# Kernel optimization log

Hardware: AMD Instinct MI355X
Metric: run time of the kernel (lower is better)

## Reference

```python
import jax, jax.numpy as jnp
import numpy as np

N_NODES = 50000
N_EDGES = 640000
D_IN = 128
D_OUT = 128


def setup_inputs() -> dict:
    key = jax.random.key(0)
    k1, k2, k3, k4, k5, k6 = jax.random.split(key, 6)
    nfeat = jax.random.normal(k1, (N_NODES, D_IN), dtype=jnp.float32)
    w = jax.random.uniform(k2, (N_EDGES,), dtype=jnp.float32)
    # nn.Linear weights are [out_feats, in_feats], Kaiming-uniform-ish scale
    bound = 1.0 / np.sqrt(D_IN)
    W1 = jax.random.uniform(k3, (D_OUT, D_IN), dtype=jnp.float32, minval=-bound, maxval=bound)
    W2 = jax.random.uniform(k4, (D_OUT, D_IN), dtype=jnp.float32, minval=-bound, maxval=bound)
    src = jax.random.randint(k5, (N_EDGES,), 0, N_NODES, dtype=jnp.int64)
    dst = jax.random.randint(k6, (N_EDGES,), 0, N_NODES, dtype=jnp.int64)
    return {"nfeat": nfeat, "w": w, "W1": W1, "W2": W2, "src": src, "dst": dst}


def reference(nfeat, w, W1, W2, src, dst):
    # feat_drop is identity in eval mode
    h = nfeat  # [N, D_IN]
    # update_all(u_mul_e('h','w','m'), sum('m','h_neighbor')):
    # gather source features, scale by per-edge scalar weight, scatter-sum to dst
    msg = h[src] * w[:, None]                                   # [E, D_IN]
    h_neighbor = jax.ops.segment_sum(msg, dst, num_segments=h.shape[0])  # [N, D_IN]
    # Bi-interaction residual: leaky_relu(Linear(h + hn)) + leaky_relu(Linear(h * hn))
    add_branch = jax.nn.leaky_relu((h + h_neighbor) @ W1.T, negative_slope=0.01)
    mul_branch = jax.nn.leaky_relu((h * h_neighbor) @ W2.T, negative_slope=0.01)
    out = add_branch + mul_branch                                # [N, D_OUT]
    return (h_neighbor, out)
```

## Files before the change

kernel.cpp:

```cpp
#include <hip/hip_runtime.h>
#include <hip/hip_bf16.h>

#define N_NODES 50000
#define N_EDGES 640000
#define D 128
#define OUT0_ELEMS (N_NODES * D)
#define SCAN_BLOCKS ((N_NODES + 255) / 256)

typedef __attribute__((ext_vector_type(8))) short short8v;
typedef __attribute__((ext_vector_type(4))) short short4v;
typedef __attribute__((ext_vector_type(4))) float f32x4;

static __device__ __forceinline__ unsigned short f2bf(float x) {
  __hip_bfloat16 b = __float2bfloat16(x);
  return *reinterpret_cast<unsigned short*>(&b);
}
static __device__ __forceinline__ float bf2f(unsigned short u) {
  unsigned x = ((unsigned)u) << 16;
  return __builtin_bit_cast(float, x);
}
static __device__ __forceinline__ unsigned pack_edge(int s, float wv) {
  return ((unsigned)f2bf(wv) << 16) | (unsigned)s;
}

__global__ __launch_bounds__(256) void conv_all(
    const float* __restrict__ nfeat, const float* __restrict__ W1,
    const float* __restrict__ W2, unsigned short* __restrict__ nf16,
    unsigned short* __restrict__ wc, int* __restrict__ cnt) {
  int i = blockIdx.x * 256 + threadIdx.x;
  int base = i * 8;
  float4 a = *(const float4*)(nfeat + base);
  float4 b = *(const float4*)(nfeat + base + 4);
  short8v o;
  o[0] = (short)f2bf(a.x); o[1] = (short)f2bf(a.y);
  o[2] = (short)f2bf(a.z); o[3] = (short)f2bf(a.w);
  o[4] = (short)f2bf(b.x); o[5] = (short)f2bf(b.y);
  o[6] = (short)f2bf(b.z); o[7] = (short)f2bf(b.w);
  *(short8v*)(nf16 + base) = o;
  if (i < D * D) {
    wc[i] = f2bf(W1[i]);
    wc[D * D + i] = f2bf(W2[i]);
  }
  if (i < N_NODES) cnt[i] = 0;
}

__global__ __launch_bounds__(256) void hist_rank(
    const int* __restrict__ dst, int* __restrict__ cnt, int* __restrict__ rank) {
  int t = blockIdx.x * 256 + threadIdx.x;
  int e = t * 4;
  if (e >= N_EDGES) return;
  int4 d4 = *(const int4*)(dst + e);
  int4 r4;
  r4.x = atomicAdd(&cnt[d4.x], 1);
  r4.y = atomicAdd(&cnt[d4.y], 1);
  r4.z = atomicAdd(&cnt[d4.z], 1);
  r4.w = atomicAdd(&cnt[d4.w], 1);
  *(int4*)(rank + e) = r4;
}

__global__ __launch_bounds__(256) void scan_block(
    const int* __restrict__ cnt, int* __restrict__ offs, int* __restrict__ bsums) {
  __shared__ int sdata[256];
  int t = threadIdx.x;
  int i = blockIdx.x * 256 + t;
  int v = (i < N_NODES) ? cnt[i] : 0;
  sdata[t] = v;
  __syncthreads();
#pragma unroll
  for (int off = 1; off < 256; off <<= 1) {
    int x = (t >= off) ? sdata[t - off] : 0;
    __syncthreads();
    sdata[t] += x;
    __syncthreads();
  }
  if (i < N_NODES) offs[i] = sdata[t] - v;
  if (t == 255) bsums[blockIdx.x] = sdata[t];
}

__global__ __launch_bounds__(256) void scan_fin(
    int* __restrict__ offs, const int* __restrict__ bsums) {
  __shared__ int sdata[256];
  int t = threadIdx.x;
  int v = (t < SCAN_BLOCKS) ? bsums[t] : 0;
  sdata[t] = v;
  __syncthreads();
#pragma unroll
  for (int off = 1; off < 256; off <<= 1) {
    int x = (t >= off) ? sdata[t - off] : 0;
    __syncthreads();
    sdata[t] += x;
    __syncthreads();
  }
  int prefix = (blockIdx.x > 0) ? sdata[blockIdx.x - 1] : 0;
  int i = blockIdx.x * 256 + t;
  if (i < N_NODES) offs[i] += prefix;
  if (i == N_NODES - 1) offs[N_NODES] = N_EDGES;
}

__global__ __launch_bounds__(256) void fill4(
    const int* __restrict__ src, const int* __restrict__ dst,
    const float* __restrict__ w, const int* __restrict__ rank,
    const int* __restrict__ offs, unsigned* __restrict__ es) {
  int t = blockIdx.x * 256 + threadIdx.x;
  int e = t * 4;
  if (e >= N_EDGES) return;
  int4 d4 = *(const int4*)(dst + e);
  int4 r4 = *(const int4*)(rank + e);
  int4 s4 = *(const int4*)(src + e);
  float4 w4 = *(const float4*)(w + e);
  es[offs[d4.x] + r4.x] = pack_edge(s4.x, w4.x);
  es[offs[d4.y] + r4.y] = pack_edge(s4.y, w4.y);
  es[offs[d4.z] + r4.z] = pack_edge(s4.z, w4.z);
  es[offs[d4.w] + r4.w] = pack_edge(s4.w, w4.w);
}

__global__ __launch_bounds__(256) void gather_bf16(
    const unsigned short* __restrict__ nf16, const int* __restrict__ offs,
    const unsigned* __restrict__ es, float* __restrict__ hn) {
  int tid = blockIdx.x * 256 + threadIdx.x;
  int node = tid >> 4;
  if (node >= N_NODES) return;
  int q = tid & 15;
  int beg = offs[node];
  int end = offs[node + 1];
  float acc[8];
#pragma unroll
  for (int j = 0; j < 8; ++j) acc[j] = 0.f;

  int k = beg;
  for (; k + 3 < end; k += 4) {
    unsigned r0 = es[k], r1 = es[k + 1], r2 = es[k + 2], r3 = es[k + 3];
    short8v v0 = *(const short8v*)(nf16 + (size_t)(r0 & 0xFFFF) * D + q * 8);
    short8v v1 = *(const short8v*)(nf16 + (size_t)(r1 & 0xFFFF) * D + q * 8);
    short8v v2 = *(const short8v*)(nf16 + (size_t)(r2 & 0xFFFF) * D + q * 8);
    short8v v3 = *(const short8v*)(nf16 + (size_t)(r3 & 0xFFFF) * D + q * 8);
    float w0 = bf2f((unsigned short)(r0 >> 16));
    float w1 = bf2f((unsigned short)(r1 >> 16));
    float w2 = bf2f((unsigned short)(r2 >> 16));
    float w3 = bf2f((unsigned short)(r3 >> 16));
#pragma unroll
    for (int j = 0; j < 8; ++j) {
      acc[j] += bf2f((unsigned short)v0[j]) * w0;
      acc[j] += bf2f((unsigned short)v1[j]) * w1;
      acc[j] += bf2f((unsigned short)v2[j]) * w2;
      acc[j] += bf2f((unsigned short)v3[j]) * w3;
    }
  }
  for (; k < end; ++k) {
    unsigned r0 = es[k];
    short8v v0 = *(const short8v*)(nf16 + (size_t)(r0 & 0xFFFF) * D + q * 8);
    float w0 = bf2f((unsigned short)(r0 >> 16));
#pragma unroll
    for (int j = 0; j < 8; ++j) acc[j] += bf2f((unsigned short)v0[j]) * w0;
  }

  float* orow = hn + (size_t)node * D + q * 8;
  *(float4*)(orow) = make_float4(acc[0], acc[1], acc[2], acc[3]);
  *(float4*)(orow + 4) = make_float4(acc[4], acc[5], acc[6], acc[7]);
}

__global__ __launch_bounds__(256) void bi_mfma_h16(
    const unsigned short* __restrict__ h16, const float* __restrict__ hn,
    const unsigned short* __restrict__ wc, float* __restrict__ out) {
  __shared__ __align__(16) unsigned short lds[2 * 64 * D];

  const int tid = threadIdx.x;
  const int lane = tid & 63;
  const int wid = tid >> 6;
  const int base = blockIdx.x * 64;
  const int r16 = lane & 15;
  const int kg = lane >> 4;

  short8v bf[2][2][4];
  {
    const int colbase = wid * 32;
#pragma unroll
    for (int g = 0; g < 2; ++g)
#pragma unroll
      for (int c = 0; c < 2; ++c)
#pragma unroll
        for (int ks = 0; ks < 4; ++ks) {
          int col = colbase + c * 16 + r16;
          int k = ks * 32 + kg * 8;
          bf[g][c][ks] =
              *(const short8v*)(wc + (size_t)g * D * D + (size_t)col * D + k);
        }
  }

#pragma unroll
  for (int p = 0; p < 8; ++p) {
    int flat = p * 1024 + tid * 4;
    int row = flat >> 7;
    int col = flat & 127;
    int node = base + row;
    float hx0 = 0.f, hx1 = 0.f, hx2 = 0.f, hx3 = 0.f;
    float4 nv = make_float4(0.f, 0.f, 0.f, 0.f);
    if (node < N_NODES) {
      short4v hv = *(const short4v*)(h16 + (size_t)node * D + col);
      hx0 = bf2f((unsigned short)hv[0]);
      hx1 = bf2f((unsigned short)hv[1]);
      hx2 = bf2f((unsigned short)hv[2]);
      hx3 = bf2f((unsigned short)hv[3]);
      nv = *(const float4*)(hn + (size_t)node * D + col);
    }
    short4v av, mv;
    av[0] = (short)f2bf(hx0 + nv.x);
    av[1] = (short)f2bf(hx1 + nv.y);
    av[2] = (short)f2bf(hx2 + nv.z);
    av[3] = (short)f2bf(hx3 + nv.w);
    mv[0] = (short)f2bf(hx0 * nv.x);
    mv[1] = (short)f2bf(hx1 * nv.y);
    mv[2] = (short)f2bf(hx2 * nv.z);
    mv[3] = (short)f2bf(hx3 * nv.w);
    int boff = (row * 256 + col * 2) ^ ((row & 7) << 4);
    *(short4v*)((char*)lds + boff) = av;
    *(short4v*)((char*)lds + 16384 + boff) = mv;
  }
  __syncthreads();

  f32x4 acc1[4][2], acc2[4][2];
#pragma unroll
  for (int rt = 0; rt < 4; ++rt)
#pragma unroll
    for (int c = 0; c < 2; ++c) {
      acc1[rt][c] = (f32x4){0.f, 0.f, 0.f, 0.f};
      acc2[rt][c] = (f32x4){0.f, 0.f, 0.f, 0.f};
    }

#pragma unroll
  for (int ks = 0; ks < 4; ++ks) {
#pragma unroll
    for (int rt = 0; rt < 4; ++rt) {
      int row = rt * 16 + r16;
      int boff = (row * 256 + (ks * 32 + kg * 8) * 2) ^ ((row & 7) << 4);
      short8v a1 = *(const short8v*)((const char*)lds + boff);
      short8v a2 = *(const short8v*)((const char*)lds + 16384 + boff);
#pragma unroll
      for (int c = 0; c < 2; ++c) {
        acc1[rt][c] = __builtin_amdgcn_mfma_f32_16x16x32_bf16(
            a1, bf[0][c][ks], acc1[rt][c], 0, 0, 0);
        acc2[rt][c] = __builtin_amdgcn_mfma_f32_16x16x32_bf16(
            a2, bf[1][c][ks], acc2[rt][c], 0, 0, 0);
      }
    }
  }

#pragma unroll
  for (int rt = 0; rt < 4; ++rt) {
#pragma unroll
    for (int c = 0; c < 2; ++c) {
#pragma unroll
      for (int e = 0; e < 4; ++e) {
        int row = rt * 16 + kg * 4 + e;
        int node = base + row;
        if (node < N_NODES) {
          int col = wid * 32 + c * 16 + r16;
          float x1 = acc1[rt][c][e];
          float x2 = acc2[rt][c][e];
          x1 = x1 > 0.f ? x1 : 0.01f * x1;
          x2 = x2 > 0.f ? x2 : 0.01f * x2;
          out[(size_t)node * D + col] = x1 + x2;
        }
      }
    }
  }
}

__global__ __launch_bounds__(256) void edge_scatter(
    const float* __restrict__ nfeat, const float* __restrict__ w,
    const int* __restrict__ src, const int* __restrict__ dst,
    float* __restrict__ hn) {
  int tid = blockIdx.x * 256 + threadIdx.x;
  int e = tid >> 5;
  if (e >= N_EDGES) return;
  int q = tid & 31;
  int s = src[e];
  int d = dst[e];
  float we = w[e];
  float4 v = ((const float4*)(nfeat + (size_t)s * D))[q];
  float* drow = hn + (size_t)d * D + q * 4;
  atomicAdd(drow + 0, v.x * we);
  atomicAdd(drow + 1, v.y * we);
  atomicAdd(drow + 2, v.z * we);
  atomicAdd(drow + 3, v.w * we);
}

__global__ __launch_bounds__(256) void bi_inter(
    const float* __restrict__ h, const float* __restrict__ hn,
    const float* __restrict__ W1, const float* __restrict__ W2,
    float* __restrict__ out) {
  int wid = __builtin_amdgcn_readfirstlane(threadIdx.x >> 6);
  int lane = threadIdx.x & 63;
  int node = blockIdx.x * 64 + lane;
  if (node >= N_NODES) return;
  const float4* h4 = (const float4*)(h + (size_t)node * D);
  const float4* n4 = (const float4*)(hn + (size_t)node * D);
  float acc1[32], acc2[32];
#pragma unroll
  for (int j = 0; j < 32; ++j) { acc1[j] = 0.f; acc2[j] = 0.f; }
  const int obase = wid * 32;
  for (int kq = 0; kq < 32; ++kq) {
    float4 hv = h4[kq];
    float4 nv = n4[kq];
    float a0 = hv.x + nv.x, a1 = hv.y + nv.y, a2 = hv.z + nv.z, a3 = hv.w + nv.w;
    float m0 = hv.x * nv.x, m1 = hv.y * nv.y, m2 = hv.z * nv.z, m3 = hv.w * nv.w;
#pragma unroll
    for (int j = 0; j < 32; ++j) {
      int o = obase + j;
      float4 w1 = *(const float4*)(W1 + (size_t)o * D + kq * 4);
      float4 w2 = *(const float4*)(W2 + (size_t)o * D + kq * 4);
      acc1[j] += a0 * w1.x + a1 * w1.y + a2 * w1.z + a3 * w1.w;
      acc2[j] += m0 * w2.x + m1 * w2.y + m2 * w2.z + m3 * w2.w;
    }
  }
  float* orow = out + (size_t)node * D + obase;
#pragma unroll
  for (int j = 0; j < 32; j += 4) {
    float4 r;
    float x;
    x = acc1[j + 0]; x = x > 0.f ? x : 0.01f * x;
    r.x = x; x = acc2[j + 0]; x = x > 0.f ? x : 0.01f * x; r.x += x;
    x = acc1[j + 1]; x = x > 0.f ? x : 0.01f * x;
    r.y = x; x = acc2[j + 1]; x = x > 0.f ? x : 0.01f * x; r.y += x;
    x = acc1[j + 2]; x = x > 0.f ? x : 0.01f * x;
    r.z = x; x = acc2[j + 2]; x = x > 0.f ? x : 0.01f * x; r.z += x;
    x = acc1[j + 3]; x = x > 0.f ? x : 0.01f * x;
    r.w = x; x = acc2[j + 3]; x = x > 0.f ? x : 0.01f * x; r.w += x;
    *(float4*)(orow + j) = r;
  }
}

extern "C" void kernel_launch(void* const* d_in, const int* in_sizes, int n_in,
                              void* d_out, int out_size, void* d_ws, size_t ws_size,
                              hipStream_t stream) {
  const float* nfeat = (const float*)d_in[0];
  const float* w     = (const float*)d_in[1];
  const float* W1    = (const float*)d_in[2];
  const float* W2    = (const float*)d_in[3];
  const int*   src   = (const int*)d_in[4];
  const int*   dst   = (const int*)d_in[5];

  float* hn  = (float*)d_out;
  float* out = (float*)d_out + OUT0_ELEMS;

  char* ws = (char*)d_ws;
  size_t off = 0;
  int* cnt = (int*)(ws + off);          off += (size_t)N_NODES * 4;
  int* offs = (int*)(ws + off);         off += (size_t)(N_NODES + 1) * 4;
  int* bsums = (int*)(ws + off);        off += 256 * 4;
  int* rank = (int*)(ws + off);         off += (size_t)N_EDGES * 4;
  unsigned* es = (unsigned*)(ws + off); off += (size_t)N_EDGES * 4;
  off = (off + 63) & ~(size_t)63;
  unsigned short* wc = (unsigned short*)(ws + off);
  off += (size_t)2 * D * D * 2;
  off = (off + 63) & ~(size_t)63;
  unsigned short* nf16 = (unsigned short*)(ws + off);
  off += (size_t)N_NODES * D * 2;
  size_t full_bytes = off;

  if (ws_size < full_bytes) {
    hipMemsetAsync(hn, 0, (size_t)OUT0_ELEMS * sizeof(float), stream);
    long long threads = (long long)N_EDGES * 32;
    int blocks = (int)((threads + 255) / 256);
    edge_scatter<<<blocks, 256, 0, stream>>>(nfeat, w, src, dst, hn);
    bi_inter<<<(N_NODES + 63) / 64, 256, 0, stream>>>(nfeat, hn, W1, W2, out);
    return;
  }

  conv_all<<<N_NODES * D / 8 / 256, 256, 0, stream>>>(
      nfeat, W1, W2, nf16, wc, cnt);
  hist_rank<<<N_EDGES / 4 / 256, 256, 0, stream>>>(dst, cnt, rank);
  scan_block<<<SCAN_BLOCKS, 256, 0, stream>>>(cnt, offs, bsums);
  scan_fin<<<SCAN_BLOCKS, 256, 0, stream>>>(offs, bsums);
  fill4<<<N_EDGES / 4 / 256, 256, 0, stream>>>(src, dst, w, rank, offs, es);
  gather_bf16<<<(N_NODES * 16 + 255) / 256, 256, 0, stream>>>(nf16, offs, es, hn);
  bi_mfma_h16<<<(N_NODES + 63) / 64, 256, 0, stream>>>(nf16, hn, wc, out);
}
```

Baseline: 109.9 us.

## Fuse gather with bi-interaction MFMA and fold block-sum scan into consumers

Result: slower. 116.1 us (+5.6%).

```diff
diff --git a/kernel.cpp b/kernel.cpp
--- a/kernel.cpp
+++ b/kernel.cpp
@@ -77,30 +77,28 @@
   if (t == 255) bsums[blockIdx.x] = sdata[t];
 }
 
-__global__ __launch_bounds__(256) void scan_fin(
-    int* __restrict__ offs, const int* __restrict__ bsums) {
-  __shared__ int sdata[256];
+static __device__ __forceinline__ void scan_bsums_lds(
+    const int* __restrict__ bsums, int* sincl) {
   int t = threadIdx.x;
   int v = (t < SCAN_BLOCKS) ? bsums[t] : 0;
-  sdata[t] = v;
+  sincl[t] = v;
   __syncthreads();
 #pragma unroll
   for (int off = 1; off < 256; off <<= 1) {
-    int x = (t >= off) ? sdata[t - off] : 0;
+    int x = (t >= off) ? sincl[t - off] : 0;
     __syncthreads();
-    sdata[t] += x;
+    sincl[t] += x;
     __syncthreads();
   }
-  int prefix = (blockIdx.x > 0) ? sdata[blockIdx.x - 1] : 0;
-  int i = blockIdx.x * 256 + t;
-  if (i < N_NODES) offs[i] += prefix;
-  if (i == N_NODES - 1) offs[N_NODES] = N_EDGES;
 }
 
 __global__ __launch_bounds__(256) void fill4(
     const int* __restrict__ src, const int* __restrict__ dst,
     const float* __restrict__ w, const int* __restrict__ rank,
-    const int* __restrict__ offs, unsigned* __restrict__ es) {
+    const int* __restrict__ offs, const int* __restrict__ bsums,
+    unsigned* __restrict__ es) {
+  __shared__ int sincl[256];
+  scan_bsums_lds(bsums, sincl);
   int t = blockIdx.x * 256 + threadIdx.x;
   int e = t * 4;
   if (e >= N_EDGES) return;
@@ -108,21 +106,41 @@
   int4 r4 = *(const int4*)(rank + e);
   int4 s4 = *(const int4*)(src + e);
   float4 w4 = *(const float4*)(w + e);
-  es[offs[d4.x] + r4.x] = pack_edge(s4.x, w4.x);
-  es[offs[d4.y] + r4.y] = pack_edge(s4.y, w4.y);
-  es[offs[d4.z] + r4.z] = pack_edge(s4.z, w4.z);
-  es[offs[d4.w] + r4.w] = pack_edge(s4.w, w4.w);
-}
-
-__global__ __launch_bounds__(256) void gather_bf16(
+  int p0 = offs[d4.x] + ((d4.x >> 8) ? sincl[(d4.x >> 8) - 1] : 0) + r4.x;
+  int p1 = offs[d4.y] + ((d4.y >> 8) ? sincl[(d4.y >> 8) - 1] : 0) + r4.y;
+  int p2 = offs[d4.z] + ((d4.z >> 8) ? sincl[(d4.z >> 8) - 1] : 0) + r4.z;
+  int p3 = offs[d4.w] + ((d4.w >> 8) ? sincl[(d4.w >> 8) - 1] : 0) + r4.w;
+  es[p0] = pack_edge(s4.x, w4.x);
+  es[p1] = pack_edge(s4.y, w4.y);
+  es[p2] = pack_edge(s4.z, w4.z);
+  es[p3] = pack_edge(s4.w, w4.w);
+}
+
+__global__ __launch_bounds__(256) void gather_bi(
     const unsigned short* __restrict__ nf16, const int* __restrict__ offs,
-    const unsigned* __restrict__ es, float* __restrict__ hn) {
-  int tid = blockIdx.x * 256 + threadIdx.x;
-  int node = tid >> 4;
-  if (node >= N_NODES) return;
-  int q = tid & 15;
-  int beg = offs[node];
-  int end = offs[node + 1];
+    const int* __restrict__ bsums, const unsigned* __restrict__ es,
+    const unsigned short* __restrict__ wc, float* __restrict__ hn,
+    float* __restrict__ out) {
+  __shared__ int sincl[256];
+  __shared__ __align__(16) unsigned short lds[2 * 16 * D];
+
+  const int tid = threadIdx.x;
+  const int base = blockIdx.x * 16;
+
+  scan_bsums_lds(bsums, sincl);
+
+  const int g = tid >> 4;
+  const int q = tid & 15;
+  const int node = base + g;
+
+  int beg = offs[node] + ((node >> 8) ? sincl[(node >> 8) - 1] : 0);
+  int end;
+  {
+    int n1 = node + 1;
+    end = (n1 == N_NODES) ? N_EDGES
+                          : offs[n1] + ((n1 >> 8) ? sincl[(n1 >> 8) - 1] : 0);
+  }
+
   float acc[8];
 #pragma unroll
   for (int j = 0; j < 8; ++j) acc[j] = 0.f;
@@ -154,114 +172,79 @@
     for (int j = 0; j < 8; ++j) acc[j] += bf2f((unsigned short)v0[j]) * w0;
   }
 
-  float* orow = hn + (size_t)node * D + q * 8;
-  *(float4*)(orow) = make_float4(acc[0], acc[1], acc[2], acc[3]);
-  *(float4*)(orow + 4) = make_float4(acc[4], acc[5], acc[6], acc[7]);
-}
-
-__global__ __launch_bounds__(256) void bi_mfma_h16(
-    const unsigned short* __restrict__ h16, const float* __restrict__ hn,
-    const unsigned short* __restrict__ wc, float* __restrict__ out) {
-  __shared__ __align__(16) unsigned short lds[2 * 64 * D];
-
-  const int tid = threadIdx.x;
+  {
+    float* orow = hn + (size_t)node * D + q * 8;
+    *(float4*)(orow) = make_float4(acc[0], acc[1], acc[2], acc[3]);
+    *(float4*)(orow + 4) = make_float4(acc[4], acc[5], acc[6], acc[7]);
+  }
+
+  {
+    short8v hv = *(const short8v*)(nf16 + (size_t)node * D + q * 8);
+    short8v av, mv;
+#pragma unroll
+    for (int j = 0; j < 8; ++j) {
+      float hx = bf2f((unsigned short)hv[j]);
+      av[j] = (short)f2bf(hx + acc[j]);
+      mv[j] = (short)f2bf(hx * acc[j]);
+    }
+    int boff = (g * 256 + q * 16) ^ ((g & 7) << 4);
+    *(short8v*)((char*)lds + boff) = av;
+    *(short8v*)((char*)lds + 4096 + boff) = mv;
+  }
+
   const int lane = tid & 63;
   const int wid = tid >> 6;
-  const int base = blockIdx.x * 64;
   const int r16 = lane & 15;
   const int kg = lane >> 4;
-
   short8v bf[2][2][4];
   {
     const int colbase = wid * 32;
 #pragma unroll
-    for (int g = 0; g < 2; ++g)
+    for (int gg = 0; gg < 2; ++gg)
 #pragma unroll
       for (int c = 0; c < 2; ++c)
 #pragma unroll
         for (int ks = 0; ks < 4; ++ks) {
           int col = colbase + c * 16 + r16;
-          int k = ks * 32 + kg * 8;
-          bf[g][c][ks] =
-              *(const short8v*)(wc + (size_t)g * D * D + (size_t)col * D + k);
+          int kk = ks * 32 + kg * 8;
+          bf[gg][c][ks] =
+              *(const short8v*)(wc + (size_t)gg * D * D + (size_t)col * D + kk);
         }
   }
-
-#pragma unroll
-  for (int p = 0; p < 8; ++p) {
-    int flat = p * 1024 + tid * 4;
-    int row = flat >> 7;
-    int col = flat & 127;
-    int node = base + row;
-    float hx0 = 0.f, hx1 = 0.f, hx2 = 0.f, hx3 = 0.f;
-    float4 nv = make_float4(0.f, 0.f, 0.f, 0.f);
-    if (node < N_NODES) {
-      short4v hv = *(const short4v*)(h16 + (size_t)node * D + col);
-      hx0 = bf2f((unsigned short)hv[0]);
-      hx1 = bf2f((unsigned short)hv[1]);
-      hx2 = bf2f((unsigned short)hv[2]);
-      hx3 = bf2f((unsigned short)hv[3]);
-      nv = *(const float4*)(hn + (size_t)node * D + col);
-    }
-    short4v av, mv;
-    av[0] = (short)f2bf(hx0 + nv.x);
-    av[1] = (short)f2bf(hx1 + nv.y);
-    av[2] = (short)f2bf(hx2 + nv.z);
-    av[3] = (short)f2bf(hx3 + nv.w);
-    mv[0] = (short)f2bf(hx0 * nv.x);
-    mv[1] = (short)f2bf(hx1 * nv.y);
-    mv[2] = (short)f2bf(hx2 * nv.z);
-    mv[3] = (short)f2bf(hx3 * nv.w);
-    int boff = (row * 256 + col * 2) ^ ((row & 7) << 4);
-    *(short4v*)((char*)lds + boff) = av;
-    *(short4v*)((char*)lds + 16384 + boff) = mv;
-  }
   __syncthreads();
 
-  f32x4 acc1[4][2], acc2[4][2];
-#pragma unroll
-  for (int rt = 0; rt < 4; ++rt)
+  f32x4 acc1[2], acc2[2];
+#pragma unroll
+  for (int c = 0; c < 2; ++c) {
+    acc1[c] = (f32x4){0.f, 0.f, 0.f, 0.f};
+    acc2[c] = (f32x4){0.f, 0.f, 0.f, 0.f};
+  }
+
+#pragma unroll
+  for (int ks = 0; ks < 4; ++ks) {
+    int boff = (r16 * 256 + (ks * 32 + kg * 8) * 2) ^ ((r16 & 7) << 4);
+    short8v a1 = *(const short8v*)((const char*)lds + boff);
+    short8v a2 = *(const short8v*)((const char*)lds + 4096 + boff);
 #pragma unroll
     for (int c = 0; c < 2; ++c) {
-      acc1[rt][c] = (f32x4){0.f, 0.f, 0.f, 0.f};
-      acc2[rt][c] = (f32x4){0.f, 0.f, 0.f, 0.f};
-    }
-
-#pragma unroll
-  for (int ks = 0; ks < 4; ++ks) {
-#pragma unroll
-    for (int rt = 0; rt < 4; ++rt) {
-      int row = rt * 16 + r16;
-      int boff = (row * 256 + (ks * 32 + kg * 8) * 2) ^ ((row & 7) << 4);
-      short8v a1 = *(const short8v*)((const char*)lds + boff);
-      short8v a2 = *(const short8v*)((const char*)lds + 16384 + boff);
-#pragma unroll
-      for (int c = 0; c < 2; ++c) {
-        acc1[rt][c] = __builtin_amdgcn_mfma_f32_16x16x32_bf16(
-            a1, bf[0][c][ks], acc1[rt][c], 0, 0, 0);
-        acc2[rt][c] = __builtin_amdgcn_mfma_f32_16x16x32_bf16(
-            a2, bf[1][c][ks], acc2[rt][c], 0, 0, 0);
-      }
-    }
-  }
-
-#pragma unroll
-  for (int rt = 0; rt < 4; ++rt) {
-#pragma unroll
-    for (int c = 0; c < 2; ++c) {
-#pragma unroll
-      for (int e = 0; e < 4; ++e) {
-        int row = rt * 16 + kg * 4 + e;
-        int node = base + row;
-        if (node < N_NODES) {
-          int col = wid * 32 + c * 16 + r16;
-          float x1 = acc1[rt][c][e];
-          float x2 = acc2[rt][c][e];
-          x1 = x1 > 0.f ? x1 : 0.01f * x1;
-          x2 = x2 > 0.f ? x2 : 0.01f * x2;
-          out[(size_t)node * D + col] = x1 + x2;
-        }
-      }
+      acc1[c] = __builtin_amdgcn_mfma_f32_16x16x32_bf16(a1, bf[0][c][ks],
+                                                        acc1[c], 0, 0, 0);
+      acc2[c] = __builtin_amdgcn_mfma_f32_16x16x32_bf16(a2, bf[1][c][ks],
+                                                        acc2[c], 0, 0, 0);
+    }
+  }
+
+#pragma unroll
+  for (int c = 0; c < 2; ++c) {
+#pragma unroll
+    for (int e = 0; e < 4; ++e) {
+      int row = kg * 4 + e;
+      int col = wid * 32 + c * 16 + r16;
+      float x1 = acc1[c][e];
+      float x2 = acc2[c][e];
+      x1 = x1 > 0.f ? x1 : 0.01f * x1;
+      x2 = x2 > 0.f ? x2 : 0.01f * x2;
+      out[(size_t)(base + row) * D + col] = x1 + x2;
     }
   }
 }
@@ -371,8 +354,8 @@
       nfeat, W1, W2, nf16, wc, cnt);
   hist_rank<<<N_EDGES / 4 / 256, 256, 0, stream>>>(dst, cnt, rank);
   scan_block<<<SCAN_BLOCKS, 256, 0, stream>>>(cnt, offs, bsums);
-  scan_fin<<<SCAN_BLOCKS, 256, 0, stream>>>(offs, bsums);
-  fill4<<<N_EDGES / 4 / 256, 256, 0, stream>>>(src, dst, w, rank, offs, es);
-  gather_bf16<<<(N_NODES * 16 + 255) / 256, 256, 0, stream>>>(nf16, offs, es, hn);
-  bi_mfma_h16<<<(N_NODES + 63) / 64, 256, 0, stream>>>(nf16, hn, wc, out);
-}
+  fill4<<<N_EDGES / 4 / 256, 256, 0, stream>>>(src, dst, w, rank, offs,
+                                               bsums, es);
+  gather_bi<<<N_NODES / 16, 256, 0, stream>>>(nf16, offs, bsums, es, wc,
+                                              hn, out);
+}
```
